# Optimization experiments

Measured on AMD Instinct MI355X. Metric: run time of the kernel, lower is better.

## Reference

```python
import jax, jax.numpy as jnp
import numpy as np

B, C, N = 16, 128, 16384


def setup_inputs() -> dict:
    key = jax.random.key(0)
    k1, k2, k3, k4, k5 = jax.random.split(key, 5)
    scale = 1.0 / np.sqrt(C)
    return {
        "feature": jax.random.normal(k1, (B, C, N), dtype=jnp.float32),
        "position": jax.random.normal(k2, (B, C, N), dtype=jnp.float32),
        "Wq": jax.random.normal(k3, (C, C), dtype=jnp.float32) * scale,
        "Wk": jax.random.normal(k4, (C, C), dtype=jnp.float32) * scale,
        "Wv": jax.random.normal(k5, (C, C), dtype=jnp.float32) * scale,
    }


def reference(feature, position, Wq, Wk, Wv):
    # 1x1 Conv1d == channel-mixing matmul: (B,C,N) x (Cout,Cin) -> (B,Cout,N)
    q = jnp.einsum("oc,bcn->bon", Wq, position)  # (B,C,N)
    k = jnp.einsum("oc,bcn->bon", Wk, position)  # (B,C,N)
    v = jnp.einsum("oc,bcn->bon", Wv, feature)   # (B,C,N)

    # torch: matmul((B,N,C,1),(B,N,1,C)).sum(dim=-2) == (sum_c q) * k
    # -> energy[b,j,n] = sq[b,n] * k[b,j,n], avoiding the (B,N,C,C) tensor.
    sq = jnp.sum(q, axis=1, keepdims=True)       # (B,1,N)
    energy = sq * k                              # (B,C,N)

    # normalize over the channel axis (torch's dim=-1 on (B,N,C) layout)
    energy = energy / (1e-9 + jnp.sum(energy, axis=1, keepdims=True))

    # softmax over channel axis (torch: Softmax(dim=1) on permuted (B,C,N))
    attention = jax.nn.softmax(energy, axis=1)   # (B,C,N)

    return attention * v + feature               # (B,C,N)
```

## Files before the change

kernel.cpp:

```cpp
#include <hip/hip_runtime.h>

#define B_ 16
#define C_ 128
#define N_ 16384
#define TN 32

typedef __attribute__((ext_vector_type(8))) short short8;
typedef __attribute__((ext_vector_type(4))) float f32x4;

__device__ inline unsigned short bf16_rn(float x) {
  unsigned u = __float_as_uint(x);
  unsigned r = u + 0x7FFFu + ((u >> 16) & 1u);
  return (unsigned short)(r >> 16);
}

__device__ inline float u16hi_f(unsigned u) { return __uint_as_float(u & 0xFFFF0000u); }
__device__ inline float u16lo_f(unsigned u) { return __uint_as_float(u << 16); }

__global__ __launch_bounds__(256) void prep_kernel(
    const float* __restrict__ Wq, const float* __restrict__ Wk, const float* __restrict__ Wv,
    float* __restrict__ wqsum,
    unsigned short* __restrict__ WkHi, unsigned short* __restrict__ WkLo,
    unsigned short* __restrict__ WvHi, unsigned short* __restrict__ WvLo) {
  int idx = blockIdx.x * 256 + threadIdx.x;
  {
    float x = Wk[idx];
    unsigned short h = bf16_rn(x);
    WkHi[idx] = h;
    WkLo[idx] = bf16_rn(x - __uint_as_float(((unsigned)h) << 16));
  }
  {
    float x = Wv[idx];
    unsigned short h = bf16_rn(x);
    WvHi[idx] = h;
    WvLo[idx] = bf16_rn(x - __uint_as_float(((unsigned)h) << 16));
  }
  if (blockIdx.x == 0 && threadIdx.x < C_) {
    int i = threadIdx.x;
    float s = 0.f;
#pragma unroll 8
    for (int o = 0; o < C_; ++o) s += Wq[o * C_ + i];
    wqsum[i] = s;
  }
}

__global__ __launch_bounds__(256, 4) void csa_mfma_kernel(
    const float* __restrict__ feature, const float* __restrict__ position,
    const float* __restrict__ wqsum,
    const unsigned short* __restrict__ WkHi, const unsigned short* __restrict__ WkLo,
    const unsigned short* __restrict__ WvHi, const unsigned short* __restrict__ WvLo,
    float* __restrict__ out) {
  __shared__ unsigned short posHi[TN * 128];
  __shared__ unsigned short posLo[TN * 128];
  __shared__ unsigned short featHi[TN * 128];
  __shared__ unsigned short featLo[TN * 128];
  __shared__ float red0[4][TN];
  __shared__ float red1[4][TN];
  __shared__ float red2[4][TN];
  __shared__ float red3[4][TN];

  const int tid = threadIdx.x;
  const int lane = tid & 63;
  const int w = tid >> 6;
  const int m = lane & 15;
  const int q = lane >> 4;
  const int b = blockIdx.x >> 9;
  const int n0 = (blockIdx.x & 511) * TN;

  const float* pos_g = position + (size_t)b * C_ * N_ + n0;
  const float* feat_g = feature + (size_t)b * C_ * N_ + n0;

  {
    const int g = tid >> 3;
    const int n4 = (tid & 7) * 4;
#pragma unroll
    for (int it = 0; it < 2; ++it) {
      int i = 64 * it + 2 * g;
      float4 p0 = *(const float4*)(pos_g + (size_t)i * N_ + n4);
      float4 p1 = *(const float4*)(pos_g + (size_t)(i + 1) * N_ + n4);
      float4 f0 = *(const float4*)(feat_g + (size_t)i * N_ + n4);
      float4 f1 = *(const float4*)(feat_g + (size_t)(i + 1) * N_ + n4);
      const float* P0 = (const float*)&p0;
      const float* P1 = (const float*)&p1;
      const float* F0 = (const float*)&f0;
      const float* F1 = (const float*)&f1;
      int c8 = (i >> 3) * 8;
      int ioff = i & 7;
#pragma unroll
      for (int d = 0; d < 4; ++d) {
        int n = n4 + d;
        int fn8 = ((n & 15) ^ ((n >> 2) & 7)) * 8;
        int hw = n * 128 + (c8 ^ fn8) + ioff;
        {
          unsigned short h0 = bf16_rn(P0[d]), h1 = bf16_rn(P1[d]);
          float l0 = P0[d] - __uint_as_float(((unsigned)h0) << 16);
          float l1 = P1[d] - __uint_as_float(((unsigned)h1) << 16);
          *(unsigned*)(posHi + hw) = (unsigned)h0 | ((unsigned)h1 << 16);
          *(unsigned*)(posLo + hw) = (unsigned)bf16_rn(l0) | ((unsigned)bf16_rn(l1) << 16);
        }
        {
          unsigned short h0 = bf16_rn(F0[d]), h1 = bf16_rn(F1[d]);
          float l0 = F0[d] - __uint_as_float(((unsigned)h0) << 16);
          float l1 = F1[d] - __uint_as_float(((unsigned)h1) << 16);
          *(unsigned*)(featHi + hw) = (unsigned)h0 | ((unsigned)h1 << 16);
          *(unsigned*)(featLo + hw) = (unsigned)bf16_rn(l0) | ((unsigned)bf16_rn(l1) << 16);
        }
      }
    }
  }
  __syncthreads();

  int rb[2], f8[2];
#pragma unroll
  for (int nt = 0; nt < 2; ++nt) {
    int n = nt * 16 + m;
    rb[nt] = n * 128;
    f8[nt] = ((n & 15) ^ ((n >> 2) & 7)) * 8;
  }

  f32x4 acck[2][2];
#pragma unroll
  for (int jt = 0; jt < 2; ++jt)
#pragma unroll
    for (int nt = 0; nt < 2; ++nt) acck[jt][nt] = (f32x4){0.f, 0.f, 0.f, 0.f};

#pragma unroll
  for (int jt = 0; jt < 2; ++jt) {
    const int arow = (32 * w + 16 * jt + m) * 128 + q * 8;
    short8 ah[4], al[4];
#pragma unroll
    for (int kk = 0; kk < 4; ++kk) {
      ah[kk] = *(const short8*)(WkHi + arow + kk * 32);
      al[kk] = *(const short8*)(WkLo + arow + kk * 32);
    }
#pragma unroll
    for (int kk = 0; kk < 4; ++kk) {
      int co = (kk * 4 + q) * 8;
      short8 bh0 = *(const short8*)(posHi + rb[0] + (co ^ f8[0]));
      short8 bl0 = *(const short8*)(posLo + rb[0] + (co ^ f8[0]));
      short8 bh1 = *(const short8*)(posHi + rb[1] + (co ^ f8[1]));
      short8 bl1 = *(const short8*)(posLo + rb[1] + (co ^ f8[1]));
      acck[jt][0] = __builtin_amdgcn_mfma_f32_16x16x32_bf16(ah[kk], bh0, acck[jt][0], 0, 0, 0);
      acck[jt][1] = __builtin_amdgcn_mfma_f32_16x16x32_bf16(ah[kk], bh1, acck[jt][1], 0, 0, 0);
      acck[jt][0] = __builtin_amdgcn_mfma_f32_16x16x32_bf16(ah[kk], bl0, acck[jt][0], 0, 0, 0);
      acck[jt][1] = __builtin_amdgcn_mfma_f32_16x16x32_bf16(ah[kk], bl1, acck[jt][1], 0, 0, 0);
      acck[jt][0] = __builtin_amdgcn_mfma_f32_16x16x32_bf16(al[kk], bh0, acck[jt][0], 0, 0, 0);
      acck[jt][1] = __builtin_amdgcn_mfma_f32_16x16x32_bf16(al[kk], bh1, acck[jt][1], 0, 0, 0);
    }
  }

  f32x4 accv[2][2];
#pragma unroll
  for (int jt = 0; jt < 2; ++jt)
#pragma unroll
    for (int nt = 0; nt < 2; ++nt) accv[jt][nt] = (f32x4){0.f, 0.f, 0.f, 0.f};

#pragma unroll
  for (int jt = 0; jt < 2; ++jt) {
    const int arow = (32 * w + 16 * jt + m) * 128 + q * 8;
    short8 ah[4], al[4];
#pragma unroll
    for (int kk = 0; kk < 4; ++kk) {
      ah[kk] = *(const short8*)(WvHi + arow + kk * 32);
      al[kk] = *(const short8*)(WvLo + arow + kk * 32);
    }
#pragma unroll
    for (int kk = 0; kk < 4; ++kk) {
      int co = (kk * 4 + q) * 8;
      short8 bh0 = *(const short8*)(featHi + rb[0] + (co ^ f8[0]));
      short8 bl0 = *(const short8*)(featLo + rb[0] + (co ^ f8[0]));
      short8 bh1 = *(const short8*)(featHi + rb[1] + (co ^ f8[1]));
      short8 bl1 = *(const short8*)(featLo + rb[1] + (co ^ f8[1]));
      accv[jt][0] = __builtin_amdgcn_mfma_f32_16x16x32_bf16(ah[kk], bh0, accv[jt][0], 0, 0, 0);
      accv[jt][1] = __builtin_amdgcn_mfma_f32_16x16x32_bf16(ah[kk], bh1, accv[jt][1], 0, 0, 0);
      accv[jt][0] = __builtin_amdgcn_mfma_f32_16x16x32_bf16(ah[kk], bl0, accv[jt][0], 0, 0, 0);
      accv[jt][1] = __builtin_amdgcn_mfma_f32_16x16x32_bf16(ah[kk], bl1, accv[jt][1], 0, 0, 0);
      accv[jt][0] = __builtin_amdgcn_mfma_f32_16x16x32_bf16(al[kk], bh0, accv[jt][0], 0, 0, 0);
      accv[jt][1] = __builtin_amdgcn_mfma_f32_16x16x32_bf16(al[kk], bh1, accv[jt][1], 0, 0, 0);
    }
  }

  float sqp[2], kp[2];
  {
    const int i0 = 32 * w + 8 * q;
    float4 wqa = *(const float4*)(wqsum + i0);
    float4 wqb = *(const float4*)(wqsum + i0 + 4);
    const int cbase = (i0 >> 3) * 8;
#pragma unroll
    for (int nt = 0; nt < 2; ++nt) {
      int hw = rb[nt] + (cbase ^ f8[nt]);
      unsigned h01 = *(const unsigned*)(posHi + hw);
      unsigned h23 = *(const unsigned*)(posHi + hw + 2);
      unsigned h45 = *(const unsigned*)(posHi + hw + 4);
      unsigned h67 = *(const unsigned*)(posHi + hw + 6);
      unsigned l01 = *(const unsigned*)(posLo + hw);
      unsigned l23 = *(const unsigned*)(posLo + hw + 2);
      unsigned l45 = *(const unsigned*)(posLo + hw + 4);
      unsigned l67 = *(const unsigned*)(posLo + hw + 6);
      float s = wqa.x * (u16lo_f(h01) + u16lo_f(l01));
      s = fmaf(wqa.y, u16hi_f(h01) + u16hi_f(l01), s);
      s = fmaf(wqa.z, u16lo_f(h23) + u16lo_f(l23), s);
      s = fmaf(wqa.w, u16hi_f(h23) + u16hi_f(l23), s);
      s = fmaf(wqb.x, u16lo_f(h45) + u16lo_f(l45), s);
      s = fmaf(wqb.y, u16hi_f(h45) + u16hi_f(l45), s);
      s = fmaf(wqb.z, u16lo_f(h67) + u16lo_f(l67), s);
      s = fmaf(wqb.w, u16hi_f(h67) + u16hi_f(l67), s);
      s += __shfl_xor(s, 16, 64);
      s += __shfl_xor(s, 32, 64);
      sqp[nt] = s;
    }
  }
#pragma unroll
  for (int nt = 0; nt < 2; ++nt) {
    float s = 0.f;
#pragma unroll
    for (int jt = 0; jt < 2; ++jt)
      s += acck[jt][nt][0] + acck[jt][nt][1] + acck[jt][nt][2] + acck[jt][nt][3];
    s += __shfl_xor(s, 16, 64);
    s += __shfl_xor(s, 32, 64);
    kp[nt] = s;
  }
  if (q == 0) {
#pragma unroll
    for (int nt = 0; nt < 2; ++nt) {
      red0[w][nt * 16 + m] = sqp[nt];
      red1[w][nt * 16 + m] = kp[nt];
    }
  }
  __syncthreads();

  float mw[2], sw[2], attscale[2];
#pragma unroll
  for (int nt = 0; nt < 2; ++nt) {
    int c = nt * 16 + m;
    float ss = red0[0][c] + red0[1][c] + red0[2][c] + red0[3][c];
    float ks = red1[0][c] + red1[1][c] + red1[2][c] + red1[3][c];
    float g = ss / (1e-9f + ss * ks);
    float mx = g * acck[0][nt][0];
#pragma unroll
    for (int jt = 0; jt < 2; ++jt)
#pragma unroll
      for (int r = 0; r < 4; ++r) mx = fmaxf(mx, g * acck[jt][nt][r]);
    mx = fmaxf(mx, __shfl_xor(mx, 16, 64));
    mx = fmaxf(mx, __shfl_xor(mx, 32, 64));
    float s = 0.f;
#pragma unroll
    for (int jt = 0; jt < 2; ++jt)
#pragma unroll
      for (int r = 0; r < 4; ++r) {
        float p = __expf(fmaf(g, acck[jt][nt][r], -mx));
        acck[jt][nt][r] = p;
        s += p;
      }
    s += __shfl_xor(s, 16, 64);
    s += __shfl_xor(s, 32, 64);
    mw[nt] = mx;
    sw[nt] = s;
  }
  if (q == 0) {
#pragma unroll
    for (int nt = 0; nt < 2; ++nt) {
      red2[w][nt * 16 + m] = mw[nt];
      red3[w][nt * 16 + m] = sw[nt];
    }
  }
  __syncthreads();
#pragma unroll
  for (int nt = 0; nt < 2; ++nt) {
    int c = nt * 16 + m;
    float M = red2[0][c];
    M = fmaxf(M, red2[1][c]);
    M = fmaxf(M, red2[2][c]);
    M = fmaxf(M, red2[3][c]);
    float es = red3[0][c] * __expf(red2[0][c] - M);
    es += red3[1][c] * __expf(red2[1][c] - M);
    es += red3[2][c] * __expf(red2[2][c] - M);
    es += red3[3][c] * __expf(red2[3][c] - M);
    attscale[nt] = __expf(mw[nt] - M) / es;
  }

  float* outp = out + (size_t)b * C_ * N_ + n0 + m;
#pragma unroll
  for (int jt = 0; jt < 2; ++jt) {
    const int jb = 32 * w + 16 * jt + 4 * q;
    const int cj = (jb >> 3) * 8;
    const int joff = jb & 7;
#pragma unroll
    for (int nt = 0; nt < 2; ++nt) {
      int hw = rb[nt] + (cj ^ f8[nt]) + joff;
      unsigned fh01 = *(const unsigned*)(featHi + hw);
      unsigned fl01 = *(const unsigned*)(featLo + hw);
      unsigned fh23 = *(const unsigned*)(featHi + hw + 2);
      unsigned fl23 = *(const unsigned*)(featLo + hw + 2);
      float fv0 = u16lo_f(fh01) + u16lo_f(fl01);
      float fv1 = u16hi_f(fh01) + u16hi_f(fl01);
      float fv2 = u16lo_f(fh23) + u16lo_f(fl23);
      float fv3 = u16hi_f(fh23) + u16hi_f(fl23);
      float as = attscale[nt];
      size_t base = (size_t)jb * N_ + nt * 16;
      outp[base] = fmaf(acck[jt][nt][0] * as, accv[jt][nt][0], fv0);
      outp[base + N_] = fmaf(acck[jt][nt][1] * as, accv[jt][nt][1], fv1);
      outp[base + (size_t)2 * N_] = fmaf(acck[jt][nt][2] * as, accv[jt][nt][2], fv2);
      outp[base + (size_t)3 * N_] = fmaf(acck[jt][nt][3] * as, accv[jt][nt][3], fv3);
    }
  }
}

extern "C" void kernel_launch(void* const* d_in, const int* in_sizes, int n_in,
                              void* d_out, int out_size, void* d_ws, size_t ws_size,
                              hipStream_t stream) {
  const float* feature = (const float*)d_in[0];
  const float* position = (const float*)d_in[1];
  const float* Wq = (const float*)d_in[2];
  const float* Wk = (const float*)d_in[3];
  const float* Wv = (const float*)d_in[4];
  float* out = (float*)d_out;

  char* ws = (char*)d_ws;
  float* wqsum = (float*)ws;
  unsigned short* WkHi = (unsigned short*)(ws + 512);
  unsigned short* WkLo = (unsigned short*)(ws + 512 + 32768);
  unsigned short* WvHi = (unsigned short*)(ws + 512 + 65536);
  unsigned short* WvLo = (unsigned short*)(ws + 512 + 98304);

  prep_kernel<<<64, 256, 0, stream>>>(Wq, Wk, Wv, wqsum, WkHi, WkLo, WvHi, WvLo);
  csa_mfma_kernel<<<B_ * (N_ / TN), 256, 0, stream>>>(feature, position, wqsum,
                                                      WkHi, WkLo, WvHi, WvLo, out);
}
```

Baseline: 422.4 us.

## Drop split-bf16 for V projection, compute sq in fp32 load, use exp2

Computes the V projection with single bf16 MFMAs instead of the hi/lo split, which removes the featLo shared buffer and the WvLo weights. The q channel-sum is now accumulated in fp32 while the inputs are loaded, and the residual feature is re-read from global memory. It also switches to hardware packed bf16 conversion and exp2-based softmax, and raises the occupancy hint to 6. The aim is less MFMA work, less LDS and VALU work, and more occupancy. The cost is lower precision in v, which may exceed the tolerance.

```diff
diff --git a/kernel.cpp b/kernel.cpp
--- a/kernel.cpp
+++ b/kernel.cpp
@@ -14,14 +14,17 @@
   return (unsigned short)(r >> 16);
 }
 
-__device__ inline float u16hi_f(unsigned u) { return __uint_as_float(u & 0xFFFF0000u); }
-__device__ inline float u16lo_f(unsigned u) { return __uint_as_float(u << 16); }
+__device__ inline unsigned cvt_pk_bf16(float a, float b) {
+  unsigned r;
+  asm("v_cvt_pk_bf16_f32 %0, %1, %2" : "=v"(r) : "v"(a), "v"(b));
+  return r;
+}
 
 __global__ __launch_bounds__(256) void prep_kernel(
     const float* __restrict__ Wq, const float* __restrict__ Wk, const float* __restrict__ Wv,
     float* __restrict__ wqsum,
     unsigned short* __restrict__ WkHi, unsigned short* __restrict__ WkLo,
-    unsigned short* __restrict__ WvHi, unsigned short* __restrict__ WvLo) {
+    unsigned short* __restrict__ WvHi) {
   int idx = blockIdx.x * 256 + threadIdx.x;
   {
     float x = Wk[idx];
@@ -29,12 +32,7 @@
     WkHi[idx] = h;
     WkLo[idx] = bf16_rn(x - __uint_as_float(((unsigned)h) << 16));
   }
-  {
-    float x = Wv[idx];
-    unsigned short h = bf16_rn(x);
-    WvHi[idx] = h;
-    WvLo[idx] = bf16_rn(x - __uint_as_float(((unsigned)h) << 16));
-  }
+  WvHi[idx] = bf16_rn(Wv[idx]);
   if (blockIdx.x == 0 && threadIdx.x < C_) {
     int i = threadIdx.x;
     float s = 0.f;
@@ -44,16 +42,15 @@
   }
 }
 
-__global__ __launch_bounds__(256, 4) void csa_mfma_kernel(
+__global__ __launch_bounds__(256, 6) void csa_mfma_kernel(
     const float* __restrict__ feature, const float* __restrict__ position,
     const float* __restrict__ wqsum,
     const unsigned short* __restrict__ WkHi, const unsigned short* __restrict__ WkLo,
-    const unsigned short* __restrict__ WvHi, const unsigned short* __restrict__ WvLo,
+    const unsigned short* __restrict__ WvHi,
     float* __restrict__ out) {
   __shared__ unsigned short posHi[TN * 128];
   __shared__ unsigned short posLo[TN * 128];
   __shared__ unsigned short featHi[TN * 128];
-  __shared__ unsigned short featLo[TN * 128];
   __shared__ float red0[4][TN];
   __shared__ float red1[4][TN];
   __shared__ float red2[4][TN];
@@ -73,6 +70,7 @@
   {
     const int g = tid >> 3;
     const int n4 = (tid & 7) * 4;
+    f32x4 sqa = (f32x4){0.f, 0.f, 0.f, 0.f};
 #pragma unroll
     for (int it = 0; it < 2; ++it) {
       int i = 64 * it + 2 * g;
@@ -80,6 +78,7 @@
       float4 p1 = *(const float4*)(pos_g + (size_t)(i + 1) * N_ + n4);
       float4 f0 = *(const float4*)(feat_g + (size_t)i * N_ + n4);
       float4 f1 = *(const float4*)(feat_g + (size_t)(i + 1) * N_ + n4);
+      float2 wq2 = *(const float2*)(wqsum + i);
       const float* P0 = (const float*)&p0;
       const float* P1 = (const float*)&p1;
       const float* F0 = (const float*)&f0;
@@ -91,21 +90,27 @@
         int n = n4 + d;
         int fn8 = ((n & 15) ^ ((n >> 2) & 7)) * 8;
         int hw = n * 128 + (c8 ^ fn8) + ioff;
-        {
-          unsigned short h0 = bf16_rn(P0[d]), h1 = bf16_rn(P1[d]);
-          float l0 = P0[d] - __uint_as_float(((unsigned)h0) << 16);
-          float l1 = P1[d] - __uint_as_float(((unsigned)h1) << 16);
-          *(unsigned*)(posHi + hw) = (unsigned)h0 | ((unsigned)h1 << 16);
-          *(unsigned*)(posLo + hw) = (unsigned)bf16_rn(l0) | ((unsigned)bf16_rn(l1) << 16);
-        }
-        {
-          unsigned short h0 = bf16_rn(F0[d]), h1 = bf16_rn(F1[d]);
-          float l0 = F0[d] - __uint_as_float(((unsigned)h0) << 16);
-          float l1 = F1[d] - __uint_as_float(((unsigned)h1) << 16);
-          *(unsigned*)(featHi + hw) = (unsigned)h0 | ((unsigned)h1 << 16);
-          *(unsigned*)(featLo + hw) = (unsigned)bf16_rn(l0) | ((unsigned)bf16_rn(l1) << 16);
-        }
+        float x0 = P0[d], x1 = P1[d];
+        unsigned hu = cvt_pk_bf16(x0, x1);
+        *(unsigned*)(posHi + hw) = hu;
+        float l0 = x0 - __uint_as_float(hu << 16);
+        float l1 = x1 - __uint_as_float(hu & 0xFFFF0000u);
+        *(unsigned*)(posLo + hw) = cvt_pk_bf16(l0, l1);
+        *(unsigned*)(featHi + hw) = cvt_pk_bf16(F0[d], F1[d]);
+        sqa[d] = fmaf(wq2.x, x0, fmaf(wq2.y, x1, sqa[d]));
       }
+    }
+#pragma unroll
+    for (int d = 0; d < 4; ++d) {
+      float s = sqa[d];
+      s += __shfl_xor(s, 8, 64);
+      s += __shfl_xor(s, 16, 64);
+      s += __shfl_xor(s, 32, 64);
+      sqa[d] = s;
+    }
+    if (lane < 8) {
+      *(float4*)&red0[w][lane * 4] =
+          make_float4(sqa[0], sqa[1], sqa[2], sqa[3]);
     }
   }
   __syncthreads();
@@ -149,67 +154,6 @@
     }
   }
 
-  f32x4 accv[2][2];
-#pragma unroll
-  for (int jt = 0; jt < 2; ++jt)
-#pragma unroll
-    for (int nt = 0; nt < 2; ++nt) accv[jt][nt] = (f32x4){0.f, 0.f, 0.f, 0.f};
-
-#pragma unroll
-  for (int jt = 0; jt < 2; ++jt) {
-    const int arow = (32 * w + 16 * jt + m) * 128 + q * 8;
-    short8 ah[4], al[4];
-#pragma unroll
-    for (int kk = 0; kk < 4; ++kk) {
-      ah[kk] = *(const short8*)(WvHi + arow + kk * 32);
-      al[kk] = *(const short8*)(WvLo + arow + kk * 32);
-    }
-#pragma unroll
-    for (int kk = 0; kk < 4; ++kk) {
-      int co = (kk * 4 + q) * 8;
-      short8 bh0 = *(const short8*)(featHi + rb[0] + (co ^ f8[0]));
-      short8 bl0 = *(const short8*)(featLo + rb[0] + (co ^ f8[0]));
-      short8 bh1 = *(const short8*)(featHi + rb[1] + (co ^ f8[1]));
-      short8 bl1 = *(const short8*)(featLo + rb[1] + (co ^ f8[1]));
-      accv[jt][0] = __builtin_amdgcn_mfma_f32_16x16x32_bf16(ah[kk], bh0, accv[jt][0], 0, 0, 0);
-      accv[jt][1] = __builtin_amdgcn_mfma_f32_16x16x32_bf16(ah[kk], bh1, accv[jt][1], 0, 0, 0);
-      accv[jt][0] = __builtin_amdgcn_mfma_f32_16x16x32_bf16(ah[kk], bl0, accv[jt][0], 0, 0, 0);
-      accv[jt][1] = __builtin_amdgcn_mfma_f32_16x16x32_bf16(ah[kk], bl1, accv[jt][1], 0, 0, 0);
-      accv[jt][0] = __builtin_amdgcn_mfma_f32_16x16x32_bf16(al[kk], bh0, accv[jt][0], 0, 0, 0);
-      accv[jt][1] = __builtin_amdgcn_mfma_f32_16x16x32_bf16(al[kk], bh1, accv[jt][1], 0, 0, 0);
-    }
-  }
-
-  float sqp[2], kp[2];
-  {
-    const int i0 = 32 * w + 8 * q;
-    float4 wqa = *(const float4*)(wqsum + i0);
-    float4 wqb = *(const float4*)(wqsum + i0 + 4);
-    const int cbase = (i0 >> 3) * 8;
-#pragma unroll
-    for (int nt = 0; nt < 2; ++nt) {
-      int hw = rb[nt] + (cbase ^ f8[nt]);
-      unsigned h01 = *(const unsigned*)(posHi + hw);
-      unsigned h23 = *(const unsigned*)(posHi + hw + 2);
-      unsigned h45 = *(const unsigned*)(posHi + hw + 4);
-      unsigned h67 = *(const unsigned*)(posHi + hw + 6);
-      unsigned l01 = *(const unsigned*)(posLo + hw);
-      unsigned l23 = *(const unsigned*)(posLo + hw + 2);
-      unsigned l45 = *(const unsigned*)(posLo + hw + 4);
-      unsigned l67 = *(const unsigned*)(posLo + hw + 6);
-      float s = wqa.x * (u16lo_f(h01) + u16lo_f(l01));
-      s = fmaf(wqa.y, u16hi_f(h01) + u16hi_f(l01), s);
-      s = fmaf(wqa.z, u16lo_f(h23) + u16lo_f(l23), s);
-      s = fmaf(wqa.w, u16hi_f(h23) + u16hi_f(l23), s);
-      s = fmaf(wqb.x, u16lo_f(h45) + u16lo_f(l45), s);
-      s = fmaf(wqb.y, u16hi_f(h45) + u16hi_f(l45), s);
-      s = fmaf(wqb.z, u16lo_f(h67) + u16lo_f(l67), s);
-      s = fmaf(wqb.w, u16hi_f(h67) + u16hi_f(l67), s);
-      s += __shfl_xor(s, 16, 64);
-      s += __shfl_xor(s, 32, 64);
-      sqp[nt] = s;
-    }
-  }
 #pragma unroll
   for (int nt = 0; nt < 2; ++nt) {
     float s = 0.f;
@@ -218,13 +162,28 @@
       s += acck[jt][nt][0] + acck[jt][nt][1] + acck[jt][nt][2] + acck[jt][nt][3];
     s += __shfl_xor(s, 16, 64);
     s += __shfl_xor(s, 32, 64);
-    kp[nt] = s;
-  }
-  if (q == 0) {
-#pragma unroll
-    for (int nt = 0; nt < 2; ++nt) {
-      red0[w][nt * 16 + m] = sqp[nt];
-      red1[w][nt * 16 + m] = kp[nt];
+    if (q == 0) red1[w][nt * 16 + m] = s;
+  }
+
+  f32x4 accv[2][2];
+#pragma unroll
+  for (int jt = 0; jt < 2; ++jt)
+#pragma unroll
+    for (int nt = 0; nt < 2; ++nt) accv[jt][nt] = (f32x4){0.f, 0.f, 0.f, 0.f};
+
+#pragma unroll
+  for (int jt = 0; jt < 2; ++jt) {
+    const int arow = (32 * w + 16 * jt + m) * 128 + q * 8;
+    short8 ah[4];
+#pragma unroll
+    for (int kk = 0; kk < 4; ++kk) ah[kk] = *(const short8*)(WvHi + arow + kk * 32);
+#pragma unroll
+    for (int kk = 0; kk < 4; ++kk) {
+      int co = (kk * 4 + q) * 8;
+      short8 bh0 = *(const short8*)(featHi + rb[0] + (co ^ f8[0]));
+      short8 bh1 = *(const short8*)(featHi + rb[1] + (co ^ f8[1]));
+      accv[jt][0] = __builtin_amdgcn_mfma_f32_16x16x32_bf16(ah[kk], bh0, accv[jt][0], 0, 0, 0);
+      accv[jt][1] = __builtin_amdgcn_mfma_f32_16x16x32_bf16(ah[kk], bh1, accv[jt][1], 0, 0, 0);
     }
   }
   __syncthreads();
@@ -235,12 +194,16 @@
     int c = nt * 16 + m;
     float ss = red0[0][c] + red0[1][c] + red0[2][c] + red0[3][c];
     float ks = red1[0][c] + red1[1][c] + red1[2][c] + red1[3][c];
-    float g = ss / (1e-9f + ss * ks);
-    float mx = g * acck[0][nt][0];
+    float gl = (ss / (1e-9f + ss * ks)) * 1.44269504f;
+    float mx = gl * acck[0][nt][0];
 #pragma unroll
     for (int jt = 0; jt < 2; ++jt)
 #pragma unroll
-      for (int r = 0; r < 4; ++r) mx = fmaxf(mx, g * acck[jt][nt][r]);
+      for (int r = 0; r < 4; ++r) {
+        float e = gl * acck[jt][nt][r];
+        acck[jt][nt][r] = e;
+        mx = fmaxf(mx, e);
+      }
     mx = fmaxf(mx, __shfl_xor(mx, 16, 64));
     mx = fmaxf(mx, __shfl_xor(mx, 32, 64));
     float s = 0.f;
@@ -248,7 +211,7 @@
     for (int jt = 0; jt < 2; ++jt)
 #pragma unroll
       for (int r = 0; r < 4; ++r) {
-        float p = __expf(fmaf(g, acck[jt][nt][r], -mx));
+        float p = exp2f(acck[jt][nt][r] - mx);
         acck[jt][nt][r] = p;
         s += p;
       }
@@ -272,32 +235,26 @@
     M = fmaxf(M, red2[1][c]);
     M = fmaxf(M, red2[2][c]);
     M = fmaxf(M, red2[3][c]);
-    float es = red3[0][c] * __expf(red2[0][c] - M);
-    es += red3[1][c] * __expf(red2[1][c] - M);
-    es += red3[2][c] * __expf(red2[2][c] - M);
-    es += red3[3][c] * __expf(red2[3][c] - M);
-    attscale[nt] = __expf(mw[nt] - M) / es;
+    float es = red3[0][c] * exp2f(red2[0][c] - M);
+    es += red3[1][c] * exp2f(red2[1][c] - M);
+    es += red3[2][c] * exp2f(red2[2][c] - M);
+    es += red3[3][c] * exp2f(red2[3][c] - M);
+    attscale[nt] = exp2f(mw[nt] - M) / es;
   }
 
   float* outp = out + (size_t)b * C_ * N_ + n0 + m;
+  const float* finp = feature + (size_t)b * C_ * N_ + n0 + m;
 #pragma unroll
   for (int jt = 0; jt < 2; ++jt) {
     const int jb = 32 * w + 16 * jt + 4 * q;
-    const int cj = (jb >> 3) * 8;
-    const int joff = jb & 7;
 #pragma unroll
     for (int nt = 0; nt < 2; ++nt) {
-      int hw = rb[nt] + (cj ^ f8[nt]) + joff;
-      unsigned fh01 = *(const unsigned*)(featHi + hw);
-      unsigned fl01 = *(const unsigned*)(featLo + hw);
-      unsigned fh23 = *(const unsigned*)(featHi + hw + 2);
-      unsigned fl23 = *(const unsigned*)(featLo + hw + 2);
-      float fv0 = u16lo_f(fh01) + u16lo_f(fl01);
-      float fv1 = u16hi_f(fh01) + u16hi_f(fl01);
-      float fv2 = u16lo_f(fh23) + u16lo_f(fl23);
-      float fv3 = u16hi_f(fh23) + u16hi_f(fl23);
       float as = attscale[nt];
       size_t base = (size_t)jb * N_ + nt * 16;
+      float fv0 = finp[base];
+      float fv1 = finp[base + N_];
+      float fv2 = finp[base + (size_t)2 * N_];
+      float fv3 = finp[base + (size_t)3 * N_];
       outp[base] = fmaf(acck[jt][nt][0] * as, accv[jt][nt][0], fv0);
       outp[base + N_] = fmaf(acck[jt][nt][1] * as, accv[jt][nt][1], fv1);
       outp[base + (size_t)2 * N_] = fmaf(acck[jt][nt][2] * as, accv[jt][nt][2], fv2);
@@ -321,9 +278,8 @@
   unsigned short* WkHi = (unsigned short*)(ws + 512);
   unsigned short* WkLo = (unsigned short*)(ws + 512 + 32768);
   unsigned short* WvHi = (unsigned short*)(ws + 512 + 65536);
-  unsigned short* WvLo = (unsigned short*)(ws + 512 + 98304);
-
-  prep_kernel<<<64, 256, 0, stream>>>(Wq, Wk, Wv, wqsum, WkHi, WkLo, WvHi, WvLo);
+
+  prep_kernel<<<64, 256, 0, stream>>>(Wq, Wk, Wv, wqsum, WkHi, WkLo, WvHi);
   csa_mfma_kernel<<<B_ * (N_ / TN), 256, 0, stream>>>(feature, position, wqsum,
-                                                      WkHi, WkLo, WvHi, WvLo, out);
-}
+                                                      WkHi, WkLo, WvHi, out);
+}
```

After: 399.0 us. -5.5%, faster.
